# Kernel optimization log

Measured on AMD Instinct MI355X. Metric: run time of the kernel, lower is better.

## Reference

```python
import jax, jax.numpy as jnp
import numpy as np

B, L, DV, DT = 64, 256, 512, 41
NT = DT - 9          # number of type-specific linears (experts)
M, V, K = 32, 64, 8  # max_seq_len, decoder vocab, template slots
TAU = 1.0            # gumbel-softmax temperature


def setup_inputs() -> dict:
    key = jax.random.key(0)
    ks = jax.random.split(key, 16)
    D2 = 2 * (DV + DT)
    inp = {}
    inp['hl'] = jax.random.normal(ks[0], (B, L, DV + DT), jnp.float32)
    inp['hr'] = jax.random.normal(ks[1], (B, L, DV + DT), jnp.float32)
    inp['cl'] = jax.random.normal(ks[2], (B, L, DV), jnp.float32)
    inp['cr'] = jax.random.normal(ks[3], (B, L, DV), jnp.float32)

    # one-hot token decodings with random lengths (token 0 = pad)
    def make_d(k):
        k1, k2 = jax.random.split(k)
        idx = jax.random.randint(k1, (B, L, M), 1, V)
        lens = jax.random.randint(k2, (B, L, 1), 1, M + 1)
        idx = jnp.where(jnp.arange(M)[None, None, :] < lens, idx, 0)
        return jax.nn.one_hot(idx, V, dtype=jnp.float32)

    inp['dl'] = make_d(ks[4])
    inp['dr'] = make_d(ks[5])
    inp['target_types'] = jax.random.randint(ks[6], (B,), 9, 9 + NT)
    inp['positions'] = jax.random.randint(ks[7], (B,), 0, L)
    s = 1.0 / np.sqrt(D2)
    inp['comp_W'] = jax.random.uniform(ks[8], (NT, D2, 5 * DV), jnp.float32, -s, s)
    inp['comp_b'] = jnp.zeros((NT, 5 * DV), jnp.float32)
    inp['tp_W1'] = jax.random.normal(ks[9], (DV, 32), jnp.float32) * 0.05
    inp['tp_b1'] = jnp.zeros((32,), jnp.float32)
    inp['tp_W2'] = jax.random.normal(ks[10], (32, 32), jnp.float32) * 0.05
    inp['tp_b2'] = jnp.zeros((32,), jnp.float32)
    inp['tp_W3'] = jax.random.normal(ks[11], (32, DT), jnp.float32) * 0.05
    inp['tp_b3'] = jnp.zeros((DT,), jnp.float32)
    inp['dec_W'] = jax.random.normal(ks[12], (NT, DV, K * 3), jnp.float32) * 0.05
    inp['dec_b'] = jnp.zeros((NT, K * 3), jnp.float32)
    inp['type_emb'] = jax.random.normal(ks[13], (DT, DV), jnp.float32)
    u = jax.random.uniform(ks[14], (B, L, DT), jnp.float32, 1e-6, 1.0 - 1e-6)
    inp['gumbel'] = -jnp.log(-jnp.log(u))  # standard Gumbel noise
    return inp


def _apply_template(codes, il, ir, len_l, len_r):
    # codes: (K,) int template codes; il, ir: (M, V); len_l/len_r: scalar int
    m = jnp.arange(M)
    e0 = jax.nn.one_hot(0, V, dtype=il.dtype)

    def step(carry, code):
        idx, done = carry
        c0 = (~done) & (code == 0) & (len_l > 0) & (idx + len_l <= M)
        c1 = (~done) & (code == 1) & (len_r > 0) & (idx + len_r <= M)
        c2 = (~done) & (code == 2) & (idx < M)
        off = jnp.clip(m - idx, 0, M - 1)
        seg0 = jnp.where(((m >= idx) & (m < idx + len_l))[:, None],
                         jnp.take(il, off, axis=0), 0.0)
        seg1 = jnp.where(((m >= idx) & (m < idx + len_r))[:, None],
                         jnp.take(ir, off, axis=0), 0.0)
        seg2 = (m == idx)[:, None].astype(il.dtype) * e0[None, :]
        out = c0 * seg0 + c1 * seg1 + c2 * seg2
        new_idx = idx + jnp.where(c0, len_l, 0) + jnp.where(c1, len_r, 0)
        return (new_idx, done | c2), out

    _, outs = jax.lax.scan(step, (jnp.int32(0), jnp.bool_(False)), codes)
    return outs.sum(0)  # (M, V)


def reference(hl, hr, cl, cr, dl, dr, target_types, positions,
              comp_W, comp_b, tp_W1, tp_b1, tp_W2, tp_b2, tp_W3, tp_b3,
              dec_W, dec_b, type_emb, gumbel):
    t = target_types - 9                                   # (B,) expert index
    hlr = jnp.concatenate([hl, hr], axis=2)                # (B, L, 2(DV+DT))
    # per-batch type-routed linear (grouped GEMM)
    v = jnp.einsum('bld,bdf->blf', hlr, comp_W[t]) + comp_b[t][:, None, :]
    i_g, fl, fr, u, o = jnp.split(v, 5, axis=2)
    c = (cl * jax.nn.sigmoid(fl + 1.0) + cr * jax.nn.sigmoid(fr + 1.0)
         + jnp.tanh(u) * jax.nn.sigmoid(i_g))
    h_v = jax.nn.sigmoid(o) * jnp.tanh(c)                  # (B, L, DV)

    # type predictor: FeedForward + gumbel-softmax (soft sample)
    h1 = jax.nn.relu(h_v @ tp_W1 + tp_b1)
    h2 = jax.nn.relu(h1 @ tp_W2 + tp_b2)
    scores = h2 @ tp_W3 + tp_b3                            # (B, L, DT)
    new_h_type = jax.nn.softmax((scores + gumbel) / TAU, axis=-1)

    # abstraction homomorphism loss: CE(log(clamp(p)), target)
    bidx = jnp.arange(B)
    sel = new_h_type[bidx, positions]                      # (B, DT)
    logp = jnp.log(jnp.clip(sel, 1e-10, 1.0))
    loss = -jnp.mean(jax.nn.log_softmax(logp, axis=-1)[bidx, target_types])

    new_h = jnp.concatenate([h_v, new_h_type], axis=2)     # (B, L, DV+DT)

    # per-type decoder template logits (same row repeated over L in torch)
    emb = type_emb[target_types]                           # (B, DV)
    dt_flat = jnp.einsum('bd,bdf->bf', emb, dec_W[t]) + dec_b[t]
    dt = jnp.broadcast_to(dt_flat.reshape(B, 1, K, 3), (B, L, K, 3))
    start_codes = jnp.full((L, K), 2).at[:, 0].set(0)
    start_tmpl = jax.nn.one_hot(start_codes, 3, dtype=jnp.float32)
    dt = jnp.where((target_types == 25)[:, None, None, None], start_tmpl[None], dt)

    dt_sample = jnp.argmax(dt, axis=-1)                    # (B, L, K)
    len_l = jnp.count_nonzero(jnp.argmax(dl, -1), axis=-1).astype(jnp.int32)
    len_r = jnp.count_nonzero(jnp.argmax(dr, -1), axis=-1).astype(jnp.int32)
    new_d = jax.vmap(jax.vmap(_apply_template))(dt_sample, dl, dr, len_l, len_r)
    return new_h, c, new_d, loss, dt
```

## Files before the change

kernel.cpp:

```cpp
#include <hip/hip_runtime.h>

#define BB 64
#define LL 256
#define DV 512
#define DT 41
#define NT 32
#define MM 32
#define VV 64
#define KK 8
#define D2 1106
#define D2P 1120
#define FIVE_DV 2560

#define OFF_NEWH 0ULL
#define OFF_C    9060352ULL
#define OFF_NEWD 17448960ULL
#define OFF_LOSS 51003392ULL
#define OFF_DT   51003393ULL

typedef __bf16 bf16x8 __attribute__((ext_vector_type(8)));
typedef float f32x4 __attribute__((ext_vector_type(4)));
typedef unsigned short u16x8 __attribute__((ext_vector_type(8)));

__device__ __forceinline__ unsigned short f2bf(float f) {
    unsigned u = __float_as_uint(f);
    u = (u + 0x7fffu + ((u >> 16) & 1u)) >> 16;
    return (unsigned short)u;
}
__device__ __forceinline__ float bf2f(unsigned short h) {
    return __uint_as_float(((unsigned)h) << 16);
}
__device__ __forceinline__ float sigm(float x) {
    return 1.0f / (1.0f + __expf(-x));
}
__device__ __forceinline__ float tanh_f(float x) {
    return 1.0f - 2.0f / (__expf(2.0f * x) + 1.0f);
}

__global__ __launch_bounds__(256) void k_hlr(const float* __restrict__ hl,
                                             const float* __restrict__ hr,
                                             unsigned short* __restrict__ hlr) {
    int row = blockIdx.x;
    int t = threadIdx.x;
    size_t sbase = (size_t)row * 553;
    size_t obase = (size_t)row * D2P;
    for (int q = 0; q < 5; ++q) {
        int k = t + q * 256;
        if (k < D2P) {
            float v = 0.0f;
            if (k < 553) v = hl[sbase + k];
            else if (k < D2) v = hr[sbase + (k - 553)];
            hlr[obase + k] = f2bf(v);
        }
    }
}

__global__ __launch_bounds__(64) void k_dec(const float* __restrict__ type_emb,
                                            const float* __restrict__ dec_W,
                                            const float* __restrict__ dec_b,
                                            const int* __restrict__ tts,
                                            int* __restrict__ codes,
                                            float* __restrict__ dtf) {
    int b = blockIdx.x;
    int t = threadIdx.x;
    int tt = tts[b];
    int e = tt - 9;
    __shared__ float dv[24];
    if (t < 24) {
        float v;
        if (tt == 25) {
            int k = t / 3, c = t % 3;
            int code = (k == 0) ? 0 : 2;
            v = (c == code) ? 1.0f : 0.0f;
        } else {
            float s = dec_b[e * 24 + t];
            const float* em = type_emb + (size_t)tt * DV;
            const float* w = dec_W + (size_t)e * DV * 24 + t;
            for (int d = 0; d < DV; ++d) s += em[d] * w[(size_t)d * 24];
            v = s;
        }
        dv[t] = v;
        dtf[b * 24 + t] = v;
    }
    __syncthreads();
    if (t < 8) {
        float b0 = dv[t * 3], b1 = dv[t * 3 + 1], b2 = dv[t * 3 + 2];
        int code = 0;
        float best = b0;
        if (b1 > best) { best = b1; code = 1; }
        if (b2 > best) { best = b2; code = 2; }
        codes[b * 8 + t] = code;
    }
}

__global__ __launch_bounds__(256, 2) void k_gemm(const unsigned short* __restrict__ hlr,
                                                 const float* __restrict__ W,
                                                 const float* __restrict__ bias,
                                                 const int* __restrict__ tts,
                                                 unsigned short* __restrict__ vws) {
    __shared__ __align__(16) unsigned short As[128 * 32];
    __shared__ __align__(16) unsigned short Bs[128 * 32];

    int b = blockIdx.z;
    int l0 = blockIdx.y * 128;
    int n0 = blockIdx.x * 128;
    int e = tts[b] - 9;
    const float* Wb = W + (size_t)e * D2 * FIVE_DV;

    int tid = threadIdx.x;
    int lane = tid & 63;
    int w = tid >> 6;
    int wr = w >> 1, wc = w & 1;
    int q = lane >> 4;
    int mr = lane & 15;

    int nB = tid & 127;
    int kg2 = tid >> 7;

    const unsigned short* Arow = hlr + (size_t)(b * LL + l0) * D2P;

    f32x4 acc[4][4];
#pragma unroll
    for (int i = 0; i < 4; ++i)
#pragma unroll
        for (int j = 0; j < 4; ++j) acc[i][j] = (f32x4)0.0f;

    for (int ks = 0; ks < 35; ++ks) {
        int k0 = ks * 32;
        __syncthreads();
#pragma unroll
        for (int i = 0; i < 2; ++i) {
            int idx = i * 256 + tid;
            int row = idx >> 2;
            int ko = (idx & 3) * 8;
            u16x8 av = *(const u16x8*)(Arow + (size_t)row * D2P + k0 + ko);
            *(u16x8*)&As[idx * 8] = av;
        }
#pragma unroll
        for (int it = 0; it < 2; ++it) {
            int kg = kg2 * 2 + it;
            int kb = kg * 8;
            u16x8 bv;
#pragma unroll
            for (int j = 0; j < 8; ++j) {
                int kk = k0 + kb + j;
                float f = (kk < D2) ? Wb[(size_t)kk * FIVE_DV + n0 + nB] : 0.0f;
                bv[j] = f2bf(f);
            }
            *(u16x8*)&Bs[nB * 32 + ((kg ^ (nB & 3)) << 3)] = bv;
        }
        __syncthreads();
        bf16x8 af[4], bfr[4];
#pragma unroll
        for (int mt = 0; mt < 4; ++mt)
            af[mt] = *(const bf16x8*)&As[(wr * 64 + mt * 16 + mr) * 32 + q * 8];
#pragma unroll
        for (int nt = 0; nt < 4; ++nt) {
            int nn = wc * 64 + nt * 16 + mr;
            bfr[nt] = *(const bf16x8*)&Bs[nn * 32 + ((q ^ (nn & 3)) << 3)];
        }
#pragma unroll
        for (int mt = 0; mt < 4; ++mt)
#pragma unroll
            for (int nt = 0; nt < 4; ++nt)
                acc[mt][nt] = __builtin_amdgcn_mfma_f32_16x16x32_bf16(
                    af[mt], bfr[nt], acc[mt][nt], 0, 0, 0);
    }

#pragma unroll
    for (int nt = 0; nt < 4; ++nt) {
        int col = n0 + wc * 64 + nt * 16 + mr;
        float bv = bias[(size_t)e * FIVE_DV + col];
#pragma unroll
        for (int mt = 0; mt < 4; ++mt) {
            int rowg = l0 + wr * 64 + mt * 16 + q * 4;
            size_t base = ((size_t)(b * LL) + rowg) * FIVE_DV + col;
#pragma unroll
            for (int r = 0; r < 4; ++r)
                vws[base + (size_t)r * FIVE_DV] = f2bf(acc[mt][nt][r] + bv);
        }
    }
}

__global__ __launch_bounds__(256) void k_cell(const unsigned short* __restrict__ vws,
                                              const float* __restrict__ cl,
                                              const float* __restrict__ cr,
                                              const float* __restrict__ W1,
                                              const float* __restrict__ b1,
                                              const float* __restrict__ W2,
                                              const float* __restrict__ b2,
                                              const float* __restrict__ W3,
                                              const float* __restrict__ b3,
                                              const float* __restrict__ gumbel,
                                              float* __restrict__ out) {
    int row = blockIdx.x;
    int t = threadIdx.x;
    __shared__ float hv[512];
    __shared__ float red[256];
    __shared__ float h1[32], h2[32], zz[41];

    const unsigned short* v = vws + (size_t)row * FIVE_DV;
    size_t c_off = OFF_C + (size_t)row * DV;
    size_t h_off = (size_t)row * 553;
    size_t cc = (size_t)row * DV;

#pragma unroll
    for (int i = 0; i < 2; ++i) {
        int j = t + i * 256;
        float ig = bf2f(v[j]);
        float fl = bf2f(v[512 + j]);
        float fr = bf2f(v[1024 + j]);
        float uu = bf2f(v[1536 + j]);
        float oo = bf2f(v[2048 + j]);
        float cv = cl[cc + j] * sigm(fl + 1.0f) + cr[cc + j] * sigm(fr + 1.0f)
                 + tanh_f(uu) * sigm(ig);
        float h = sigm(oo) * tanh_f(cv);
        out[c_off + j] = cv;
        out[h_off + j] = h;
        hv[j] = h;
    }
    __syncthreads();
    {
        int jj = t & 31, g = t >> 5;
        float p = 0.0f;
        int d0 = g * 64;
        for (int d = d0; d < d0 + 64; ++d) p += hv[d] * W1[d * 32 + jj];
        red[t] = p;
    }
    __syncthreads();
    if (t < 32) {
        float s = b1[t];
#pragma unroll
        for (int g = 0; g < 8; ++g) s += red[g * 32 + t];
        h1[t] = s > 0.0f ? s : 0.0f;
    }
    __syncthreads();
    if (t < 32) {
        float s = b2[t];
        for (int d = 0; d < 32; ++d) s += h1[d] * W2[d * 32 + t];
        h2[t] = s > 0.0f ? s : 0.0f;
    }
    __syncthreads();
    if (t < 41) {
        float s = b3[t];
        for (int d = 0; d < 32; ++d) s += h2[d] * W3[d * 41 + t];
        zz[t] = s + gumbel[(size_t)row * DT + t];
    }
    __syncthreads();
    if (t < 64) {
        float val = (t < 41) ? zz[t] : -3.4e38f;
        float m = val;
        for (int off = 32; off; off >>= 1) m = fmaxf(m, __shfl_xor(m, off, 64));
        float ex = (t < 41) ? __expf(val - m) : 0.0f;
        float s = ex;
        for (int off = 32; off; off >>= 1) s += __shfl_xor(s, off, 64);
        if (t < 41) out[h_off + 512 + t] = ex / s;
    }
}

__global__ __launch_bounds__(64) void k_loss(const float* __restrict__ out,
                                             const int* __restrict__ positions,
                                             const int* __restrict__ tts,
                                             float* __restrict__ loss_out) {
    int b = threadIdx.x;
    int pos = positions[b];
    int tt = tts[b];
    size_t base = ((size_t)(b * LL + pos)) * 553 + 512;
    float mx = -3.4e38f;
    float lp_t = 0.0f;
    float lps[41];
    for (int i = 0; i < 41; ++i) {
        float p = out[base + i];
        p = fminf(fmaxf(p, 1e-10f), 1.0f);
        float lp = __logf(p);
        lps[i] = lp;
        mx = fmaxf(mx, lp);
        if (i == tt) lp_t = lp;
    }
    float s = 0.0f;
    for (int i = 0; i < 41; ++i) s += __expf(lps[i] - mx);
    float lse = mx + __logf(s);
    float val = lp_t - lse;
    float a = -val / 64.0f;
    for (int off = 32; off; off >>= 1) a += __shfl_xor(a, off, 64);
    if (b == 0) *loss_out = a;
}

__global__ __launch_bounds__(256) void k_newd(const float* __restrict__ dl,
                                              const float* __restrict__ dr,
                                              const int* __restrict__ codes,
                                              const float* __restrict__ dtf,
                                              float* __restrict__ newd,
                                              float* __restrict__ dtout) {
    int row = blockIdx.x;
    int t = threadIdx.x;
    int b = row >> 8;
    __shared__ int sT[32];
    __shared__ int sO[32];
    __shared__ int lens[2];
    __shared__ int cds[8];

    if (t < 2) lens[t] = 0;
    if (t < 32) sT[t] = 0;
    if (t < 8) cds[t] = codes[b * 8 + t];
    __syncthreads();
    size_t dbase = (size_t)row * (MM * VV);
    if (t < 32) {
        if (dl[dbase + (size_t)t * VV] < 0.5f) atomicAdd(&lens[0], 1);
        if (dr[dbase + (size_t)t * VV] < 0.5f) atomicAdd(&lens[1], 1);
    }
    __syncthreads();
    if (t == 0) {
        int idx = 0;
        bool done = false;
        int ll = lens[0], lr = lens[1];
        for (int k = 0; k < 8; ++k) {
            int code = cds[k];
            if (done) continue;
            if (code == 0) {
                if (ll > 0 && idx + ll <= MM) {
                    for (int m = 0; m < ll; ++m) { sT[idx + m] = 1; sO[idx + m] = m; }
                    idx += ll;
                }
            } else if (code == 1) {
                if (lr > 0 && idx + lr <= MM) {
                    for (int m = 0; m < lr; ++m) { sT[idx + m] = 2; sO[idx + m] = m; }
                    idx += lr;
                }
            } else {
                if (idx < MM) { sT[idx] = 3; done = true; }
            }
        }
    }
    __syncthreads();
#pragma unroll
    for (int rep = 0; rep < 2; ++rep) {
        int e4 = t + rep * 256;
        int m = e4 >> 4, v4 = e4 & 15;
        int st = sT[m];
        float4 val = {0.0f, 0.0f, 0.0f, 0.0f};
        if (st == 1) val = *(const float4*)(dl + dbase + (size_t)sO[m] * VV + v4 * 4);
        else if (st == 2) val = *(const float4*)(dr + dbase + (size_t)sO[m] * VV + v4 * 4);
        else if (st == 3 && v4 == 0) val.x = 1.0f;
        *(float4*)(newd + dbase + (size_t)e4 * 4) = val;
    }
    if (t < 24) dtout[(size_t)row * 24 + t] = dtf[b * 24 + t];
}

extern "C" void kernel_launch(void* const* d_in, const int* in_sizes, int n_in,
                              void* d_out, int out_size, void* d_ws, size_t ws_size,
                              hipStream_t stream) {
    const float* hl = (const float*)d_in[0];
    const float* hr = (const float*)d_in[1];
    const float* cl = (const float*)d_in[2];
    const float* cr = (const float*)d_in[3];
    const float* dl = (const float*)d_in[4];
    const float* dr = (const float*)d_in[5];
    const int* target_types = (const int*)d_in[6];
    const int* positions = (const int*)d_in[7];
    const float* comp_W = (const float*)d_in[8];
    const float* comp_b = (const float*)d_in[9];
    const float* tp_W1 = (const float*)d_in[10];
    const float* tp_b1 = (const float*)d_in[11];
    const float* tp_W2 = (const float*)d_in[12];
    const float* tp_b2 = (const float*)d_in[13];
    const float* tp_W3 = (const float*)d_in[14];
    const float* tp_b3 = (const float*)d_in[15];
    const float* dec_W = (const float*)d_in[16];
    const float* dec_b = (const float*)d_in[17];
    const float* type_emb = (const float*)d_in[18];
    const float* gumbel = (const float*)d_in[19];

    float* out = (float*)d_out;

    const size_t HLR_BYTES = (size_t)BB * LL * D2P * 2;
    unsigned short* hlr = (unsigned short*)d_ws;
    int* codes = (int*)((char*)d_ws + HLR_BYTES);
    float* dtf = (float*)((char*)d_ws + HLR_BYTES + 2048);

    unsigned short* vws = (unsigned short*)(out + OFF_NEWD);

    k_hlr<<<BB * LL, 256, 0, stream>>>(hl, hr, hlr);
    k_dec<<<BB, 64, 0, stream>>>(type_emb, dec_W, dec_b, target_types, codes, dtf);
    k_gemm<<<dim3(FIVE_DV / 128, LL / 128, BB), 256, 0, stream>>>(
        hlr, comp_W, comp_b, target_types, vws);
    k_cell<<<BB * LL, 256, 0, stream>>>(vws, cl, cr, tp_W1, tp_b1, tp_W2, tp_b2,
                                        tp_W3, tp_b3, gumbel, out);
    k_loss<<<1, 64, 0, stream>>>(out, positions, target_types, out + OFF_LOSS);
    k_newd<<<BB * LL, 256, 0, stream>>>(dl, dr, codes, dtf, out + OFF_NEWD,
                                        out + OFF_DT);
}
```

Baseline: 1.131 ms.

## Pre-transpose expert weights to bf16 and stream GEMM tiles via global_load_lds

Adds a kernel that converts and transposes all 32 expert weight matrices into a K-contiguous bf16 layout in workspace. A new GEMM then loads both operand tiles straight into swizzled LDS with 16-byte global_load_lds, avoiding the strided per-element fp32 weight loads and in-loop conversion. It also vectorises the cell kernel's gate and state loads. In exchange it converts every expert's weights on each call, including those no batch selects, and depends on enough workspace, falling back to the old GEMM otherwise.

Result: slower. 1.197 ms (+5.8%).

```diff
diff --git a/kernel.cpp b/kernel.cpp
--- a/kernel.cpp
+++ b/kernel.cpp
@@ -9,7 +9,7 @@
 #define VV 64
 #define KK 8
 #define D2 1106
-#define D2P 1120
+#define KP 1120
 #define FIVE_DV 2560
 
 #define OFF_NEWH 0ULL
@@ -35,6 +35,12 @@
 }
 __device__ __forceinline__ float tanh_f(float x) {
     return 1.0f - 2.0f / (__expf(2.0f * x) + 1.0f);
+}
+
+__device__ __forceinline__ void gll16(void* lds, const void* g) {
+    __builtin_amdgcn_global_load_lds(
+        (const __attribute__((address_space(1))) unsigned int*)g,
+        (__attribute__((address_space(3))) unsigned int*)lds, 16, 0, 0);
 }
 
 __global__ __launch_bounds__(256) void k_hlr(const float* __restrict__ hl,
@@ -43,16 +49,44 @@
     int row = blockIdx.x;
     int t = threadIdx.x;
     size_t sbase = (size_t)row * 553;
-    size_t obase = (size_t)row * D2P;
+    size_t obase = (size_t)row * KP;
     for (int q = 0; q < 5; ++q) {
         int k = t + q * 256;
-        if (k < D2P) {
+        if (k < KP) {
             float v = 0.0f;
             if (k < 553) v = hl[sbase + k];
             else if (k < D2) v = hr[sbase + (k - 553)];
             hlr[obase + k] = f2bf(v);
         }
     }
+}
+
+__global__ __launch_bounds__(256) void k_wconv(const float* __restrict__ W,
+                                               unsigned short* __restrict__ Wt) {
+    __shared__ float tile[32][33];
+    int e = blockIdx.z;
+    int k0 = blockIdx.y * 32;
+    int n0 = blockIdx.x * 32;
+    int t = threadIdx.x;
+    int c = t & 31;
+    int r0 = (t >> 5) * 4;
+#pragma unroll
+    for (int rr = 0; rr < 4; ++rr) {
+        int r = r0 + rr;
+        int k = k0 + r;
+        float v = 0.0f;
+        if (k < D2) v = W[((size_t)e * D2 + k) * FIVE_DV + n0 + c];
+        tile[c][r] = v;
+    }
+    __syncthreads();
+    int rn = t >> 3;
+    int ck0 = (t & 7) * 4;
+    ushort4 o;
+    o.x = f2bf(tile[rn][ck0]);
+    o.y = f2bf(tile[rn][ck0 + 1]);
+    o.z = f2bf(tile[rn][ck0 + 2]);
+    o.w = f2bf(tile[rn][ck0 + 3]);
+    *(ushort4*)&Wt[((size_t)e * FIVE_DV + n0 + rn) * KP + k0 + ck0] = o;
 }
 
 __global__ __launch_bounds__(64) void k_dec(const float* __restrict__ type_emb,
@@ -93,6 +127,85 @@
     }
 }
 
+__global__ __launch_bounds__(256, 2) void k_gemm2(const unsigned short* __restrict__ hlr,
+                                                  const unsigned short* __restrict__ Wt,
+                                                  const float* __restrict__ bias,
+                                                  const int* __restrict__ tts,
+                                                  unsigned short* __restrict__ vws) {
+    __shared__ __align__(16) unsigned short As[128 * 32];
+    __shared__ __align__(16) unsigned short Bs[128 * 32];
+
+    int b = blockIdx.z;
+    int l0 = blockIdx.y * 128;
+    int n0 = blockIdx.x * 128;
+    int e = tts[b] - 9;
+
+    int tid = threadIdx.x;
+    int lane = tid & 63;
+    int w = tid >> 6;
+    int wr = w >> 1, wc = w & 1;
+    int q = lane >> 4;
+    int mr = lane & 15;
+
+    const unsigned short* Abase = hlr + (size_t)(b * LL + l0) * KP;
+    const unsigned short* Bbase = Wt + ((size_t)e * FIVE_DV + n0) * KP;
+
+    size_t soff[2];
+#pragma unroll
+    for (int i = 0; i < 2; ++i) {
+        int chunk = w * 128 + i * 64 + lane;
+        int row = chunk >> 2;
+        int kc = (chunk & 3) ^ (row & 3);
+        soff[i] = (size_t)row * KP + kc * 8;
+    }
+    int swz = (q ^ (mr & 3)) << 3;
+
+    f32x4 acc[4][4];
+#pragma unroll
+    for (int i = 0; i < 4; ++i)
+#pragma unroll
+        for (int j = 0; j < 4; ++j) acc[i][j] = (f32x4)0.0f;
+
+    for (int ks = 0; ks < 35; ++ks) {
+        int k0 = ks * 32;
+        __syncthreads();
+#pragma unroll
+        for (int i = 0; i < 2; ++i) {
+            int lbase = (w * 128 + i * 64) * 8;
+            gll16(&As[lbase], Abase + soff[i] + k0);
+            gll16(&Bs[lbase], Bbase + soff[i] + k0);
+        }
+        __syncthreads();
+        bf16x8 af[4], bfr[4];
+#pragma unroll
+        for (int mt = 0; mt < 4; ++mt)
+            af[mt] = *(const bf16x8*)&As[(wr * 64 + mt * 16 + mr) * 32 + swz];
+#pragma unroll
+        for (int nt = 0; nt < 4; ++nt)
+            bfr[nt] = *(const bf16x8*)&Bs[(wc * 64 + nt * 16 + mr) * 32 + swz];
+#pragma unroll
+        for (int mt = 0; mt < 4; ++mt)
+#pragma unroll
+            for (int nt = 0; nt < 4; ++nt)
+                acc[mt][nt] = __builtin_amdgcn_mfma_f32_16x16x32_bf16(
+                    af[mt], bfr[nt], acc[mt][nt], 0, 0, 0);
+    }
+
+#pragma unroll
+    for (int nt = 0; nt < 4; ++nt) {
+        int col = n0 + wc * 64 + nt * 16 + mr;
+        float bv = bias[(size_t)e * FIVE_DV + col];
+#pragma unroll
+        for (int mt = 0; mt < 4; ++mt) {
+            int rowg = l0 + wr * 64 + mt * 16 + q * 4;
+            size_t base = ((size_t)(b * LL) + rowg) * FIVE_DV + col;
+#pragma unroll
+            for (int r = 0; r < 4; ++r)
+                vws[base + (size_t)r * FIVE_DV] = f2bf(acc[mt][nt][r] + bv);
+        }
+    }
+}
+
 __global__ __launch_bounds__(256, 2) void k_gemm(const unsigned short* __restrict__ hlr,
                                                  const float* __restrict__ W,
                                                  const float* __restrict__ bias,
@@ -117,7 +230,7 @@
     int nB = tid & 127;
     int kg2 = tid >> 7;
 
-    const unsigned short* Arow = hlr + (size_t)(b * LL + l0) * D2P;
+    const unsigned short* Arow = hlr + (size_t)(b * LL + l0) * KP;
 
     f32x4 acc[4][4];
 #pragma unroll
@@ -133,7 +246,7 @@
             int idx = i * 256 + tid;
             int row = idx >> 2;
             int ko = (idx & 3) * 8;
-            u16x8 av = *(const u16x8*)(Arow + (size_t)row * D2P + k0 + ko);
+            u16x8 av = *(const u16x8*)(Arow + (size_t)row * KP + k0 + ko);
             *(u16x8*)&As[idx * 8] = av;
         }
 #pragma unroll
@@ -204,20 +317,31 @@
     size_t h_off = (size_t)row * 553;
     size_t cc = (size_t)row * DV;
 
-#pragma unroll
-    for (int i = 0; i < 2; ++i) {
-        int j = t + i * 256;
-        float ig = bf2f(v[j]);
-        float fl = bf2f(v[512 + j]);
-        float fr = bf2f(v[1024 + j]);
-        float uu = bf2f(v[1536 + j]);
-        float oo = bf2f(v[2048 + j]);
-        float cv = cl[cc + j] * sigm(fl + 1.0f) + cr[cc + j] * sigm(fr + 1.0f)
-                 + tanh_f(uu) * sigm(ig);
-        float h = sigm(oo) * tanh_f(cv);
-        out[c_off + j] = cv;
-        out[h_off + j] = h;
-        hv[j] = h;
+    {
+        int j = 2 * t;
+        unsigned int pig = *(const unsigned int*)&v[j];
+        unsigned int pfl = *(const unsigned int*)&v[512 + j];
+        unsigned int pfr = *(const unsigned int*)&v[1024 + j];
+        unsigned int puu = *(const unsigned int*)&v[1536 + j];
+        unsigned int poo = *(const unsigned int*)&v[2048 + j];
+        float2 clv = *(const float2*)&cl[cc + j];
+        float2 crv = *(const float2*)&cr[cc + j];
+#pragma unroll
+        for (int i = 0; i < 2; ++i) {
+            float ig = bf2f((unsigned short)(i ? (pig >> 16) : (pig & 0xffff)));
+            float fl = bf2f((unsigned short)(i ? (pfl >> 16) : (pfl & 0xffff)));
+            float fr = bf2f((unsigned short)(i ? (pfr >> 16) : (pfr & 0xffff)));
+            float uu = bf2f((unsigned short)(i ? (puu >> 16) : (puu & 0xffff)));
+            float oo = bf2f((unsigned short)(i ? (poo >> 16) : (poo & 0xffff)));
+            float cli = i ? clv.y : clv.x;
+            float cri = i ? crv.y : crv.x;
+            float cv = cli * sigm(fl + 1.0f) + cri * sigm(fr + 1.0f)
+                     + tanh_f(uu) * sigm(ig);
+            float h = sigm(oo) * tanh_f(cv);
+            out[c_off + j + i] = cv;
+            out[h_off + j + i] = h;
+            hv[j + i] = h;
+        }
     }
     __syncthreads();
     {
@@ -373,17 +497,28 @@
 
     float* out = (float*)d_out;
 
-    const size_t HLR_BYTES = (size_t)BB * LL * D2P * 2;
+    const size_t HLR_BYTES = (size_t)BB * LL * KP * 2;
+    const size_t WT_OFF = HLR_BYTES + 8192;
+    const size_t WT_BYTES = (size_t)NT * FIVE_DV * KP * 2;
     unsigned short* hlr = (unsigned short*)d_ws;
     int* codes = (int*)((char*)d_ws + HLR_BYTES);
     float* dtf = (float*)((char*)d_ws + HLR_BYTES + 2048);
+    unsigned short* Wt = (unsigned short*)((char*)d_ws + WT_OFF);
 
     unsigned short* vws = (unsigned short*)(out + OFF_NEWD);
 
     k_hlr<<<BB * LL, 256, 0, stream>>>(hl, hr, hlr);
     k_dec<<<BB, 64, 0, stream>>>(type_emb, dec_W, dec_b, target_types, codes, dtf);
-    k_gemm<<<dim3(FIVE_DV / 128, LL / 128, BB), 256, 0, stream>>>(
-        hlr, comp_W, comp_b, target_types, vws);
+
+    if (ws_size >= WT_OFF + WT_BYTES) {
+        k_wconv<<<dim3(80, 35, 32), 256, 0, stream>>>(comp_W, Wt);
+        k_gemm2<<<dim3(FIVE_DV / 128, LL / 128, BB), 256, 0, stream>>>(
+            hlr, Wt, comp_b, target_types, vws);
+    } else {
+        k_gemm<<<dim3(FIVE_DV / 128, LL / 128, BB), 256, 0, stream>>>(
+            hlr, comp_W, comp_b, target_types, vws);
+    }
+
     k_cell<<<BB * LL, 256, 0, stream>>>(vws, cl, cr, tp_W1, tp_b1, tp_W2, tp_b2,
                                         tp_W3, tp_b3, gumbel, out);
     k_loss<<<1, 64, 0, stream>>>(out, positions, target_types, out + OFF_LOSS);
```

## Cover full L per GEMM block, load A via global_load_lds, vectorize W loads

Applied to the files above, without the earlier changes.

The expert GEMM now assigns each block all 256 rows of a batch, as two 128-row halves sharing one converted B tile. This halves the fp32 weight reads and bf16 conversions per output. A tiles are moved straight into swizzled LDS with global_load_lds, and W is read as float4 rows and packed into bf16 pairs under a new swizzle. The cell kernel reads its bf16 pairs and c values with wider loads. In exchange the grid is half as large (1280 blocks) and there are twice as many accumulator registers, which may reduce occupancy.

Measured after the change: 1.057 ms. 1.07x faster.

```diff
diff --git a/kernel.cpp b/kernel.cpp
--- a/kernel.cpp
+++ b/kernel.cpp
@@ -1,4 +1,5 @@
 #include <hip/hip_runtime.h>
+#include <hip/hip_bf16.h>
 
 #define BB 64
 #define LL 256
@@ -9,7 +10,7 @@
 #define VV 64
 #define KK 8
 #define D2 1106
-#define D2P 1120
+#define KP 1120
 #define FIVE_DV 2560
 
 #define OFF_NEWH 0ULL
@@ -27,6 +28,9 @@
     u = (u + 0x7fffu + ((u >> 16) & 1u)) >> 16;
     return (unsigned short)u;
 }
+__device__ __forceinline__ unsigned pack2bf(float a, float b) {
+    return (unsigned)f2bf(a) | ((unsigned)f2bf(b) << 16);
+}
 __device__ __forceinline__ float bf2f(unsigned short h) {
     return __uint_as_float(((unsigned)h) << 16);
 }
@@ -35,6 +39,12 @@
 }
 __device__ __forceinline__ float tanh_f(float x) {
     return 1.0f - 2.0f / (__expf(2.0f * x) + 1.0f);
+}
+
+__device__ __forceinline__ void gll16(void* lds, const void* g) {
+    __builtin_amdgcn_global_load_lds(
+        (const __attribute__((address_space(1))) unsigned int*)g,
+        (__attribute__((address_space(3))) unsigned int*)lds, 16, 0, 0);
 }
 
 __global__ __launch_bounds__(256) void k_hlr(const float* __restrict__ hl,
@@ -43,10 +53,10 @@
     int row = blockIdx.x;
     int t = threadIdx.x;
     size_t sbase = (size_t)row * 553;
-    size_t obase = (size_t)row * D2P;
+    size_t obase = (size_t)row * KP;
     for (int q = 0; q < 5; ++q) {
         int k = t + q * 256;
-        if (k < D2P) {
+        if (k < KP) {
             float v = 0.0f;
             if (k < 553) v = hl[sbase + k];
             else if (k < D2) v = hr[sbase + (k - 553)];
@@ -93,16 +103,15 @@
     }
 }
 
-__global__ __launch_bounds__(256, 2) void k_gemm(const unsigned short* __restrict__ hlr,
-                                                 const float* __restrict__ W,
-                                                 const float* __restrict__ bias,
-                                                 const int* __restrict__ tts,
-                                                 unsigned short* __restrict__ vws) {
-    __shared__ __align__(16) unsigned short As[128 * 32];
+__global__ __launch_bounds__(256, 2) void k_gemmF(const unsigned short* __restrict__ hlr,
+                                                  const float* __restrict__ W,
+                                                  const float* __restrict__ bias,
+                                                  const int* __restrict__ tts,
+                                                  unsigned short* __restrict__ vws) {
+    __shared__ __align__(16) unsigned short As[2][128 * 32];
     __shared__ __align__(16) unsigned short Bs[128 * 32];
 
-    int b = blockIdx.z;
-    int l0 = blockIdx.y * 128;
+    int b = blockIdx.y;
     int n0 = blockIdx.x * 128;
     int e = tts[b] - 9;
     const float* Wb = W + (size_t)e * D2 * FIVE_DV;
@@ -114,57 +123,82 @@
     int q = lane >> 4;
     int mr = lane & 15;
 
-    int nB = tid & 127;
-    int kg2 = tid >> 7;
-
-    const unsigned short* Arow = hlr + (size_t)(b * LL + l0) * D2P;
-
-    f32x4 acc[4][4];
-#pragma unroll
-    for (int i = 0; i < 4; ++i)
-#pragma unroll
-        for (int j = 0; j < 4; ++j) acc[i][j] = (f32x4)0.0f;
+    const unsigned short* Abase = hlr + (size_t)(b * LL) * KP;
+
+    size_t soff[2];
+#pragma unroll
+    for (int i = 0; i < 2; ++i) {
+        int chunk = w * 128 + i * 64 + lane;
+        int row = chunk >> 2;
+        int kc = (chunk & 3) ^ (row & 3);
+        soff[i] = (size_t)row * KP + kc * 8;
+    }
+    int swzA = (q ^ (mr & 3)) << 3;
+
+    int r = tid >> 5;
+    int nb = (tid & 31) * 4;
+    int kcw = r >> 1;
+    int koffw = (r & 1) * 4;
+
+    f32x4 acc[2][4][4];
+#pragma unroll
+    for (int h = 0; h < 2; ++h)
+#pragma unroll
+        for (int i = 0; i < 4; ++i)
+#pragma unroll
+            for (int j = 0; j < 4; ++j) acc[h][i][j] = (f32x4)0.0f;
 
     for (int ks = 0; ks < 35; ++ks) {
         int k0 = ks * 32;
         __syncthreads();
 #pragma unroll
-        for (int i = 0; i < 2; ++i) {
-            int idx = i * 256 + tid;
-            int row = idx >> 2;
-            int ko = (idx & 3) * 8;
-            u16x8 av = *(const u16x8*)(Arow + (size_t)row * D2P + k0 + ko);
-            *(u16x8*)&As[idx * 8] = av;
-        }
-#pragma unroll
-        for (int it = 0; it < 2; ++it) {
-            int kg = kg2 * 2 + it;
-            int kb = kg * 8;
-            u16x8 bv;
-#pragma unroll
-            for (int j = 0; j < 8; ++j) {
-                int kk = k0 + kb + j;
-                float f = (kk < D2) ? Wb[(size_t)kk * FIVE_DV + n0 + nB] : 0.0f;
-                bv[j] = f2bf(f);
+        for (int h = 0; h < 2; ++h)
+#pragma unroll
+            for (int i = 0; i < 2; ++i) {
+                int lbase = (w * 128 + i * 64) * 8;
+                gll16(&As[h][lbase], Abase + (size_t)h * 128 * KP + soff[i] + k0);
             }
-            *(u16x8*)&Bs[nB * 32 + ((kg ^ (nB & 3)) << 3)] = bv;
+        {
+            float4 f[4];
+#pragma unroll
+            for (int i = 0; i < 4; ++i) {
+                int kg = k0 + 4 * r + i;
+                if (kg < D2)
+                    f[i] = *(const float4*)(Wb + (size_t)kg * FIVE_DV + n0 + nb);
+                else
+                    f[i] = make_float4(0.f, 0.f, 0.f, 0.f);
+            }
+#pragma unroll
+            for (int j = 0; j < 4; ++j) {
+                int n = nb + j;
+                int s = (n & 3) ^ ((n >> 2) & 3);
+                uint2 pk;
+                pk.x = pack2bf(((const float*)&f[0])[j], ((const float*)&f[1])[j]);
+                pk.y = pack2bf(((const float*)&f[2])[j], ((const float*)&f[3])[j]);
+                *(uint2*)&Bs[n * 32 + ((kcw ^ s) << 3) + koffw] = pk;
+            }
         }
         __syncthreads();
-        bf16x8 af[4], bfr[4];
-#pragma unroll
-        for (int mt = 0; mt < 4; ++mt)
-            af[mt] = *(const bf16x8*)&As[(wr * 64 + mt * 16 + mr) * 32 + q * 8];
+        bf16x8 bfr[4];
 #pragma unroll
         for (int nt = 0; nt < 4; ++nt) {
-            int nn = wc * 64 + nt * 16 + mr;
-            bfr[nt] = *(const bf16x8*)&Bs[nn * 32 + ((q ^ (nn & 3)) << 3)];
-        }
-#pragma unroll
-        for (int mt = 0; mt < 4; ++mt)
-#pragma unroll
-            for (int nt = 0; nt < 4; ++nt)
-                acc[mt][nt] = __builtin_amdgcn_mfma_f32_16x16x32_bf16(
-                    af[mt], bfr[nt], acc[mt][nt], 0, 0, 0);
+            int n = wc * 64 + nt * 16 + mr;
+            int s = (n & 3) ^ ((n >> 2) & 3);
+            bfr[nt] = *(const bf16x8*)&Bs[n * 32 + ((q ^ s) << 3)];
+        }
+#pragma unroll
+        for (int h = 0; h < 2; ++h) {
+            bf16x8 af[4];
+#pragma unroll
+            for (int mt = 0; mt < 4; ++mt)
+                af[mt] = *(const bf16x8*)&As[h][(wr * 64 + mt * 16 + mr) * 32 + swzA];
+#pragma unroll
+            for (int mt = 0; mt < 4; ++mt)
+#pragma unroll
+                for (int nt = 0; nt < 4; ++nt)
+                    acc[h][mt][nt] = __builtin_amdgcn_mfma_f32_16x16x32_bf16(
+                        af[mt], bfr[nt], acc[h][mt][nt], 0, 0, 0);
+        }
     }
 
 #pragma unroll
@@ -172,13 +206,15 @@
         int col = n0 + wc * 64 + nt * 16 + mr;
         float bv = bias[(size_t)e * FIVE_DV + col];
 #pragma unroll
-        for (int mt = 0; mt < 4; ++mt) {
-            int rowg = l0 + wr * 64 + mt * 16 + q * 4;
-            size_t base = ((size_t)(b * LL) + rowg) * FIVE_DV + col;
-#pragma unroll
-            for (int r = 0; r < 4; ++r)
-                vws[base + (size_t)r * FIVE_DV] = f2bf(acc[mt][nt][r] + bv);
-        }
+        for (int h = 0; h < 2; ++h)
+#pragma unroll
+            for (int mt = 0; mt < 4; ++mt) {
+                int rowg = h * 128 + wr * 64 + mt * 16 + q * 4;
+                size_t base = ((size_t)(b * LL) + rowg) * FIVE_DV + col;
+#pragma unroll
+                for (int rr = 0; rr < 4; ++rr)
+                    vws[base + (size_t)rr * FIVE_DV] = f2bf(acc[h][mt][nt][rr] + bv);
+            }
     }
 }
 
@@ -204,20 +240,31 @@
     size_t h_off = (size_t)row * 553;
     size_t cc = (size_t)row * DV;
 
-#pragma unroll
-    for (int i = 0; i < 2; ++i) {
-        int j = t + i * 256;
-        float ig = bf2f(v[j]);
-        float fl = bf2f(v[512 + j]);
-        float fr = bf2f(v[1024 + j]);
-        float uu = bf2f(v[1536 + j]);
-        float oo = bf2f(v[2048 + j]);
-        float cv = cl[cc + j] * sigm(fl + 1.0f) + cr[cc + j] * sigm(fr + 1.0f)
-                 + tanh_f(uu) * sigm(ig);
-        float h = sigm(oo) * tanh_f(cv);
-        out[c_off + j] = cv;
-        out[h_off + j] = h;
-        hv[j] = h;
+    {
+        int j = 2 * t;
+        unsigned int pig = *(const unsigned int*)&v[j];
+        unsigned int pfl = *(const unsigned int*)&v[512 + j];
+        unsigned int pfr = *(const unsigned int*)&v[1024 + j];
+        unsigned int puu = *(const unsigned int*)&v[1536 + j];
+        unsigned int poo = *(const unsigned int*)&v[2048 + j];
+        float2 clv = *(const float2*)&cl[cc + j];
+        float2 crv = *(const float2*)&cr[cc + j];
+#pragma unroll
+        for (int i = 0; i < 2; ++i) {
+            float ig = bf2f((unsigned short)(i ? (pig >> 16) : (pig & 0xffff)));
+            float fl = bf2f((unsigned short)(i ? (pfl >> 16) : (pfl & 0xffff)));
+            float fr = bf2f((unsigned short)(i ? (pfr >> 16) : (pfr & 0xffff)));
+            float uu = bf2f((unsigned short)(i ? (puu >> 16) : (puu & 0xffff)));
+            float oo = bf2f((unsigned short)(i ? (poo >> 16) : (poo & 0xffff)));
+            float cli = i ? clv.y : clv.x;
+            float cri = i ? crv.y : crv.x;
+            float cv = cli * sigm(fl + 1.0f) + cri * sigm(fr + 1.0f)
+                     + tanh_f(uu) * sigm(ig);
+            float h = sigm(oo) * tanh_f(cv);
+            out[c_off + j + i] = cv;
+            out[h_off + j + i] = h;
+            hv[j + i] = h;
+        }
     }
     __syncthreads();
     {
@@ -373,7 +420,7 @@
 
     float* out = (float*)d_out;
 
-    const size_t HLR_BYTES = (size_t)BB * LL * D2P * 2;
+    const size_t HLR_BYTES = (size_t)BB * LL * KP * 2;
     unsigned short* hlr = (unsigned short*)d_ws;
     int* codes = (int*)((char*)d_ws + HLR_BYTES);
     float* dtf = (float*)((char*)d_ws + HLR_BYTES + 2048);
@@ -382,7 +429,7 @@
 
     k_hlr<<<BB * LL, 256, 0, stream>>>(hl, hr, hlr);
     k_dec<<<BB, 64, 0, stream>>>(type_emb, dec_W, dec_b, target_types, codes, dtf);
-    k_gemm<<<dim3(FIVE_DV / 128, LL / 128, BB), 256, 0, stream>>>(
+    k_gemmF<<<dim3(FIVE_DV / 128, BB), 256, 0, stream>>>(
         hlr, comp_W, comp_b, target_types, vws);
     k_cell<<<BB * LL, 256, 0, stream>>>(vws, cl, cr, tp_W1, tp_b1, tp_W2, tp_b2,
                                         tp_W3, tp_b3, gumbel, out);
```
